# Kernel optimization log

Measured on AMD Instinct MI355X. Metric: run time of the kernel, lower is better.

Reference implementation:

```python
import jax, jax.numpy as jnp
import numpy as np
from jax import lax

EPS = 1e-6

def _class_wise_pool(x, g):
    # torch ClassWisePool: average groups of g consecutive channels
    b, c, h, w = x.shape
    return x.reshape(b, c // g, g, h, w).mean(axis=2)

def _conv1x1(wgt, bias, t):
    return jnp.einsum('oi,bihw->bohw', wgt, t) + bias[None, :, None, None]

def setup_inputs() -> dict:
    key = jax.random.key(0)
    ks = jax.random.split(key, 13)
    B, H, W = 64, 14, 14
    f = lambda k, s, sc=1.0: jax.random.normal(k, s, dtype=jnp.float32) * sc
    return {
        'r5': f(ks[0], (B, 2048, H, W)),
        'fc0_w': f(ks[1], (512, 2048, 3, 3), 0.01),
        'bn_gamma': 1.0 + 0.1 * f(ks[2], (512,)),
        'bn_beta': 0.1 * f(ks[3], (512,)),
        'bn_mean': 0.1 * f(ks[4], (512,)),
        'bn_var': 0.5 + jax.random.uniform(ks[5], (512,), dtype=jnp.float32),
        'mu0': f(ks[6], (512, 8)),
        'conv4_w': f(ks[7], (2048, 4096), 0.02),
        'conv4_b': jnp.zeros((2048,), jnp.float32),
        'down_w': f(ks[8], (32, 2048), 0.02),
        'down_b': jnp.zeros((32,), jnp.float32),
        'cls_w': f(ks[9], (8, 4096), 0.02),
        'cls_b': jnp.zeros((8,), jnp.float32),
    }

def reference(r5, fc0_w, bn_gamma, bn_beta, bn_mean, bn_var, mu0,
              conv4_w, conv4_b, down_w, down_b, cls_w, cls_b):
    B, _, H, W = r5.shape
    N = H * W
    K = 8  # emotional categories

    # fc0: Conv3x3 -> BN(eval) -> ReLU, 2048 -> 512
    y = lax.conv_general_dilated(r5, fc0_w, (1, 1), ((1, 1), (1, 1)),
                                 dimension_numbers=('NCHW', 'OIHW', 'NCHW'))
    y = (y - bn_mean[:, None, None]) * (bn_gamma / jnp.sqrt(bn_var + 1e-5))[:, None, None] + bn_beta[:, None, None]
    y = jax.nn.relu(y)

    # CAE / EM attention (EMANet-style), stage_num = 3
    x = y.reshape(B, 512, N)
    mu = mu0 / (jnp.linalg.norm(mu0, axis=0, keepdims=True) + EPS)  # [512, K]
    mu = jnp.broadcast_to(mu[None], (B, 512, K))
    z = None
    for _ in range(3):
        z = jax.nn.softmax(jnp.einsum('bcn,bck->bnk', x, mu), axis=-1)  # [B,N,K]
        zn = z / (z.sum(axis=1, keepdims=True) + EPS)
        mu = jnp.einsum('bcn,bnk->bck', x, zn)
        mu = mu / (jnp.linalg.norm(mu, axis=1, keepdims=True) + EPS)
    x_r = jnp.einsum('bck,bnk->bcn', mu, z)
    x2 = jax.nn.relu(x + x_r).reshape(B, 512, H, W)  # GCEM output
    z_t = z.transpose(0, 2, 1).reshape(B, K, H, W)   # attention map

    # class_att = z_t.view(b,8,1,h,w).mean(2) == z_t
    # per-class matmul loop + 8 cats -> single einsum, channel order i-major
    x1 = jnp.einsum('bchw,bkwv->bkchv', x2, z_t).reshape(B, K * 512, H, W)

    dic_global = _conv1x1(conv4_w, conv4_b, x1)             # [B,2048,H,W]
    xb = jnp.concatenate([r5 * dic_global, r5], axis=1)     # [B,4096,H,W]
    xb = _conv1x1(conv4_w, conv4_b, xb)                     # same conv4 reused

    xd = _conv1x1(down_w, down_b, xb)                       # downconv [B,32,H,W]
    xg = _class_wise_pool(xd.mean(axis=(2, 3), keepdims=True), 4).reshape(B, 8)  # GAP + pool
    xc = _class_wise_pool(xd, 4) * xg[:, :, None, None]     # [B,8,H,W]
    xc = _class_wise_pool(xc, 8)                            # [B,1,H,W]

    # 2047 sequential torch.cat == broadcast to 2048 channels
    xcopy = jnp.broadcast_to(xc, (B, 2048, H, W)) * r5
    xcopy = jnp.concatenate([r5, xcopy], axis=1).mean(axis=(2, 3))  # GAP -> [B,4096]
    out2 = xcopy @ cls_w.T + cls_b
    return (xg, out2)
```

## Files before the change

kernel.cpp:

```cpp
#include <hip/hip_runtime.h>
#include <hip/hip_bf16.h>

typedef unsigned short u16;
typedef unsigned int   u32;
typedef __attribute__((ext_vector_type(4))) float f32x4;
typedef __attribute__((ext_vector_type(8))) short s16x8;

__device__ __forceinline__ float b2f(u16 u){ u32 x = ((u32)u) << 16; return __builtin_bit_cast(float, x); }
__device__ __forceinline__ u16 f2b(float f){
  u32 x = __builtin_bit_cast(u32, f);
  u32 r = (x + 0x7FFFu + ((x >> 16) & 1u)) >> 16;
  return (u16)r;
}
__device__ __forceinline__ float inld(const void* p, size_t i, int isbf){
  return isbf ? b2f(((const u16*)p)[i]) : ((const float*)p)[i];
}
__device__ __forceinline__ u16 inld16(const void* p, size_t i, int isbf){
  return isbf ? ((const u16*)p)[i] : f2b(((const float*)p)[i]);
}

__global__ __launch_bounds__(256) void detect_kernel(const u32* __restrict__ r5w, int* __restrict__ flag){
  __shared__ int cnt[2];
  int t = threadIdx.x;
  if (t < 2) cnt[t] = 0;
  __syncthreads();
  int inw = 0, nz = 0;
  for (int i = t; i < 16384; i += 256){
    u32 w = r5w[i];
    if (w == 0u) continue;
    u32 e = (w >> 7) & 0xFFu;
    nz++;
    if (e >= 0x58u && e <= 0x98u) inw++;
  }
  atomicAdd(&cnt[0], inw);
  atomicAdd(&cnt[1], nz);
  __syncthreads();
  if (t == 0) flag[0] = (2 * cnt[0] >= cnt[1]) ? 1 : 0;
}

__global__ __launch_bounds__(256) void prep_kernel(
    const void* __restrict__ g, const void* __restrict__ be,
    const void* __restrict__ mn, const void* __restrict__ vr,
    const void* __restrict__ dw, const void* __restrict__ db,
    const void* __restrict__ b4, const int* __restrict__ flag,
    float* __restrict__ scale, float* __restrict__ bias,
    u16* __restrict__ dwp, float* __restrict__ dbp,
    u16* __restrict__ b4c, u16* __restrict__ zrow)
{
  const int isbf = *flag;
  int idx = blockIdx.x * 256 + threadIdx.x;
  if (idx < 512){
    float s = inld(g, idx, isbf) / sqrtf(inld(vr, idx, isbf) + 1e-5f);
    scale[idx] = s;
    bias[idx]  = inld(be, idx, isbf) - inld(mn, idx, isbf) * s;
  }
  if (idx < 128) dbp[idx] = (idx < 32) ? inld(db, idx, isbf) : 0.f;
  if (idx < 2048){
    zrow[idx] = 0;
    b4c[idx] = inld16(b4, idx, isbf);
  }
  if (idx < 128 * 2048){
    int j = idx >> 11;
    dwp[idx] = (j < 32) ? inld16(dw, idx, isbf) : (u16)0;
  }
}

__global__ __launch_bounds__(256) void wt_pack(const void* __restrict__ w, const int* __restrict__ flag,
                                               u16* __restrict__ wt){
  const int isbf = *flag;
  int idx = blockIdx.x * 256 + threadIdx.x;
  if (idx >= 512 * 18432) return;
  int o = idx / 18432;
  int r = idx - o * 18432;
  int tap = r >> 11, i = r & 2047;
  wt[idx] = inld16(w, ((size_t)(o * 2048 + i)) * 9 + tap, isbf);
}

__global__ __launch_bounds__(256) void cvt_w4(const void* __restrict__ w4, const int* __restrict__ flag,
                                              u16* __restrict__ w4c){
  const int isbf = *flag;
  int idx = blockIdx.x * 256 + threadIdx.x;
  if (idx < 2048 * 4096) w4c[idx] = inld16(w4, idx, isbf);
}

__global__ __launch_bounds__(256) void transpose_r5(const void* __restrict__ r5, size_t elem_off,
                                                    const int* __restrict__ flag, u16* __restrict__ r5nk){
  __shared__ u16 tile[64 * 197];
  const int isbf = *flag;
  int blk = blockIdx.x;
  int b = blk >> 5, c0 = (blk & 31) * 64;
  int t = threadIdx.x;
  size_t src = elem_off + ((size_t)b * 2048 + c0) * 196;
  for (int q = t; q < 64 * 196; q += 256){
    int cl = q / 196, hv = q - cl * 196;
    tile[cl * 197 + hv] = inld16(r5, src + q, isbf);
  }
  __syncthreads();
  for (int q = t; q < 64 * 196; q += 256){
    int hv = q >> 6, cl = q & 63;
    r5nk[((size_t)b * 196 + hv) * 2048 + c0 + cl] = tile[cl * 197 + hv];
  }
}

template<int MODE>
__global__ __launch_bounds__(256) void gemm_bt(
    const u16* __restrict__ Aptr, const u16* __restrict__ A2,
    const u16* __restrict__ Bw, void* __restrict__ Cout,
    const float* __restrict__ sc, const float* __restrict__ bi,
    const u16* __restrict__ bias16, const u16* __restrict__ zrow,
    int K, int ldA, int Mrows)
{
  __shared__ u16 As[128 * 32];
  __shared__ u16 Bs[128 * 32];
  const int tid = threadIdx.x;
  const int wv = tid >> 6, ln = tid & 63;
  const int m0 = blockIdx.x * 128;
  const int o0 = blockIdx.y * 128;

  const int row0 = tid >> 2;
  const int row1 = row0 + 64;
  const int kk = (tid & 3) * 8;

  int mAr[2];
  mAr[0] = m0 + row0; mAr[1] = m0 + row1;
  #pragma unroll
  for (int s = 0; s < 2; s++) if (mAr[s] >= Mrows) mAr[s] = Mrows - 1;

  int hA[2], vA[2];
  if constexpr (MODE == 0){
    #pragma unroll
    for (int s = 0; s < 2; s++){
      int hv = mAr[s] % 196;
      hA[s] = hv / 14; vA[s] = hv - hA[s] * 14;
    }
  }
  const u16* Brow0 = Bw + (size_t)(o0 + row0) * K + kk;
  const u16* Brow1 = Bw + (size_t)(o0 + row1) * K + kk;

  const int wm = (wv >> 1) * 64, wn = (wv & 1) * 64;
  const int fl = ln & 15, fq = ln >> 4;

  f32x4 acc[4][4];
  #pragma unroll
  for (int i = 0; i < 4; i++)
    #pragma unroll
    for (int j = 0; j < 4; j++) acc[i][j] = (f32x4){0.f, 0.f, 0.f, 0.f};

  for (int k0 = 0; k0 < K; k0 += 32){
    const u16 *ga0, *ga1;
    if constexpr (MODE == 0){
      int tap = k0 >> 11;
      int kin = (k0 & 2047) + kk;
      int dy = tap / 3 - 1, dx = tap - (tap / 3) * 3 - 1;
      int dlt = dy * 14 + dx;
      bool ok0 = ((unsigned)(hA[0] + dy) < 14u) && ((unsigned)(vA[0] + dx) < 14u);
      bool ok1 = ((unsigned)(hA[1] + dy) < 14u) && ((unsigned)(vA[1] + dx) < 14u);
      ga0 = ok0 ? Aptr + (size_t)(mAr[0] + dlt) * 2048 + kin : zrow + kk;
      ga1 = ok1 ? Aptr + (size_t)(mAr[1] + dlt) * 2048 + kin : zrow + kk;
    } else if constexpr (MODE == 2){
      const u16* base = (k0 < 2048) ? Aptr : A2;
      int kin = (k0 & 2047) + kk;
      ga0 = base + (size_t)mAr[0] * 2048 + kin;
      ga1 = base + (size_t)mAr[1] * 2048 + kin;
    } else {
      ga0 = Aptr + (size_t)mAr[0] * ldA + k0 + kk;
      ga1 = Aptr + (size_t)mAr[1] * ldA + k0 + kk;
    }
    uint4 a0 = *(const uint4*)ga0;
    uint4 a1 = *(const uint4*)ga1;
    uint4 b0 = *(const uint4*)(Brow0 + k0);
    uint4 b1 = *(const uint4*)(Brow1 + k0);

    __syncthreads();
    *(uint4*)&As[row0 * 32 + kk] = a0;
    *(uint4*)&As[row1 * 32 + kk] = a1;
    *(uint4*)&Bs[row0 * 32 + kk] = b0;
    *(uint4*)&Bs[row1 * 32 + kk] = b1;
    __syncthreads();

    s16x8 af[4], bfr[4];
    #pragma unroll
    for (int i = 0; i < 4; i++)
      af[i] = *(const s16x8*)&As[(wm + i * 16 + fl) * 32 + fq * 8];
    #pragma unroll
    for (int j = 0; j < 4; j++)
      bfr[j] = *(const s16x8*)&Bs[(wn + j * 16 + fl) * 32 + fq * 8];
    #pragma unroll
    for (int i = 0; i < 4; i++)
      #pragma unroll
      for (int j = 0; j < 4; j++)
        acc[i][j] = __builtin_amdgcn_mfma_f32_16x16x32_bf16(af[i], bfr[j], acc[i][j], 0, 0, 0);
  }

  #pragma unroll
  for (int i = 0; i < 4; i++){
    int mrow = m0 + wm + i * 16 + fq * 4;
    #pragma unroll
    for (int j = 0; j < 4; j++){
      int o = o0 + wn + j * 16 + fl;
      f32x4 a = acc[i][j];
      #pragma unroll
      for (int r = 0; r < 4; r++){
        int n = mrow + r;
        if (n >= Mrows) continue;
        float v = a[r];
        if constexpr (MODE == 0){
          v = fmaxf(v * sc[o] + bi[o], 0.f);
          ((u16*)Cout)[(size_t)n * 512 + o] = f2b(v);
        } else if constexpr (MODE == 1){
          v += b2f(bias16[o]);
          v *= b2f(A2[(size_t)n * 2048 + o]);
          ((u16*)Cout)[(size_t)n * 2048 + o] = f2b(v);
        } else if constexpr (MODE == 2){
          v += b2f(bias16[o]);
          ((u16*)Cout)[(size_t)n * 2048 + o] = f2b(v);
        } else {
          ((float*)Cout)[(size_t)n * 128 + o] = v + bi[o];
        }
      }
    }
  }
}

__global__ __launch_bounds__(512) void em_kernel(
    const u16* __restrict__ x, const void* __restrict__ mu0, const int* __restrict__ flag,
    u16* __restrict__ x2, float* __restrict__ zg)
{
  __shared__ float mu[512][8];
  __shared__ float zz[196][8];
  __shared__ float part[64][8];
  __shared__ float red8[8];
  const int isbf = *flag;
  const int b = blockIdx.x;
  const int t = threadIdx.x;
  const u16* xb = x + (size_t)b * 196 * 512;

  for (int q = t; q < 4096; q += 512) mu[q >> 3][q & 7] = inld(mu0, q, isbf);
  __syncthreads();
  { int k = t & 7, g = t >> 3; float s = 0;
    for (int c = g; c < 512; c += 64){ float m = mu[c][k]; s += m * m; }
    part[g][k] = s; }
  __syncthreads();
  if (t < 8){ float s = 0; for (int g = 0; g < 64; g++) s += part[g][t]; red8[t] = sqrtf(s) + 1e-6f; }
  __syncthreads();
  for (int q = t; q < 4096; q += 512) mu[q >> 3][q & 7] /= red8[q & 7];
  __syncthreads();

  for (int it = 0; it < 3; it++){
    for (int p = t; p < 1568; p += 512){
      int n = p >> 3, k = p & 7;
      const u16* xr = xb + n * 512;
      float s = 0;
      for (int c = 0; c < 512; c += 8){
        uint4 u = *(const uint4*)(xr + c);
        s += b2f((u16)(u.x & 0xffff)) * mu[c][k]     + b2f((u16)(u.x >> 16)) * mu[c + 1][k]
           + b2f((u16)(u.y & 0xffff)) * mu[c + 2][k] + b2f((u16)(u.y >> 16)) * mu[c + 3][k]
           + b2f((u16)(u.z & 0xffff)) * mu[c + 4][k] + b2f((u16)(u.z >> 16)) * mu[c + 5][k]
           + b2f((u16)(u.w & 0xffff)) * mu[c + 6][k] + b2f((u16)(u.w >> 16)) * mu[c + 7][k];
      }
      zz[n][k] = s;
    }
    __syncthreads();
    if (t < 196){
      float mx = zz[t][0];
      #pragma unroll
      for (int k = 1; k < 8; k++) mx = fmaxf(mx, zz[t][k]);
      float e[8], sm = 0;
      #pragma unroll
      for (int k = 0; k < 8; k++){ e[k] = expf(zz[t][k] - mx); sm += e[k]; }
      #pragma unroll
      for (int k = 0; k < 8; k++) zz[t][k] = e[k] / sm;
    }
    __syncthreads();
    { int k = t & 7, g = t >> 3; float s = 0;
      for (int n = g; n < 196; n += 64) s += zz[n][k];
      part[g][k] = s; }
    __syncthreads();
    if (t < 8){ float s = 0; for (int g = 0; g < 64; g++) s += part[g][t]; red8[t] = s + 1e-6f; }
    __syncthreads();
    for (int q = t; q < 4096; q += 512){
      int c = q >> 3, k = q & 7;
      float s = 0;
      for (int n = 0; n < 196; n++) s += b2f(xb[n * 512 + c]) * zz[n][k];
      mu[c][k] = s / red8[k];
    }
    __syncthreads();
    { int k = t & 7, g = t >> 3; float s = 0;
      for (int c = g; c < 512; c += 64){ float m = mu[c][k]; s += m * m; }
      part[g][k] = s; }
    __syncthreads();
    if (t < 8){ float s = 0; for (int g = 0; g < 64; g++) s += part[g][t]; red8[t] = sqrtf(s) + 1e-6f; }
    __syncthreads();
    for (int q = t; q < 4096; q += 512) mu[q >> 3][q & 7] /= red8[q & 7];
    __syncthreads();
  }

  for (int p = t; p < 1568; p += 512) zg[b * 1568 + p] = zz[p >> 3][p & 7];
  for (int q = t; q < 196 * 512; q += 512){
    int n = q >> 9, c = q & 511;
    float xr = 0;
    #pragma unroll
    for (int k = 0; k < 8; k++) xr += mu[c][k] * zz[n][k];
    float v = b2f(xb[n * 512 + c]) + xr;
    x2[(size_t)b * 196 * 512 + q] = f2b(fmaxf(v, 0.f));
  }
}

__global__ __launch_bounds__(256) void expand_kernel(
    const u16* __restrict__ x2, const float* __restrict__ zg, u16* __restrict__ x1)
{
  __shared__ u16 xs[14 * 512];
  __shared__ float zb[196 * 8];
  int bh = blockIdx.x;
  int b = bh / 14, h = bh - b * 14;
  int t = threadIdx.x;
  const u16* src = x2 + ((size_t)b * 196 + h * 14) * 512;
  for (int q = t; q < 14 * 512; q += 256) xs[q] = src[q];
  for (int q = t; q < 1568; q += 256) zb[q] = zg[b * 1568 + q];
  __syncthreads();
  size_t outbase = ((size_t)b * 196 + h * 14) * 4096;
  for (int q = t; q < 14 * 4096; q += 256){
    int v = q >> 12, kc = q & 4095;
    int k = kc >> 9, c = kc & 511;
    float s = 0;
    #pragma unroll
    for (int w = 0; w < 14; w++)
      s += b2f(xs[w * 512 + c]) * zb[(w * 14 + v) * 8 + k];
    x1[outbase + q] = f2b(s);
  }
}

__global__ __launch_bounds__(256) void pool_xg(
    const float* __restrict__ xd, const int* __restrict__ flag,
    float* __restrict__ g32, void* __restrict__ outbase, int elem_off)
{
  __shared__ float part[8][32];
  int b = blockIdx.x, t = threadIdx.x;
  int j = t & 31, g = t >> 5;
  float s = 0;
  for (int hv = g; hv < 196; hv += 8)
    s += xd[((size_t)b * 196 + hv) * 128 + j];
  part[g][j] = s;
  __syncthreads();
  if (t < 32){
    float s2 = 0;
    #pragma unroll
    for (int g2 = 0; g2 < 8; g2++) s2 += part[g2][t];
    part[0][t] = s2 * (1.f / 196.f);
  }
  __syncthreads();
  if (t < 8){
    float v = 0.25f * (part[0][4 * t] + part[0][4 * t + 1] + part[0][4 * t + 2] + part[0][4 * t + 3]);
    g32[b * 8 + t] = v;
    int o = elem_off + b * 8 + t;
    if (*flag) ((u16*)outbase)[o] = f2b(v);
    else       ((float*)outbase)[o] = v;
  }
}

__global__ __launch_bounds__(256) void final_kernel(
    const float* __restrict__ xd, const float* __restrict__ g32,
    const u16* __restrict__ r5nk, const void* __restrict__ clsw,
    const void* __restrict__ clsb, const int* __restrict__ flag,
    void* __restrict__ outbase, int elem_off)
{
  __shared__ float xc[196];
  __shared__ float red[8];
  const int isbf = *flag;
  int b = blockIdx.x, t = threadIdx.x;
  if (t < 196){
    float s = 0;
    const float* row = xd + ((size_t)b * 196 + t) * 128;
    #pragma unroll
    for (int j = 0; j < 32; j++) s += row[j] * g32[b * 8 + (j >> 2)];
    xc[t] = s * (1.f / 32.f);
  }
  if (t < 8) red[t] = 0.f;
  __syncthreads();
  float s1[8], s2[8];
  #pragma unroll
  for (int ci = 0; ci < 8; ci++){ s1[ci] = 0.f; s2[ci] = 0.f; }
  for (int hv = 0; hv < 196; hv++){
    const u16* row = r5nk + ((size_t)b * 196 + hv) * 2048;
    float xcv = xc[hv];
    #pragma unroll
    for (int ci = 0; ci < 8; ci++){
      float v = b2f(row[t + ci * 256]);
      s1[ci] += v; s2[ci] += v * xcv;
    }
  }
  float pm[8];
  #pragma unroll
  for (int m = 0; m < 8; m++) pm[m] = 0.f;
  #pragma unroll
  for (int ci = 0; ci < 8; ci++){
    int c = t + ci * 256;
    float a1 = s1[ci] * (1.f / 196.f), a2 = s2[ci] * (1.f / 196.f);
    #pragma unroll
    for (int m = 0; m < 8; m++)
      pm[m] += inld(clsw, m * 4096 + c, isbf) * a1 + inld(clsw, m * 4096 + 2048 + c, isbf) * a2;
  }
  #pragma unroll
  for (int m = 0; m < 8; m++) atomicAdd(&red[m], pm[m]);
  __syncthreads();
  if (t < 8){
    float v = red[t] + inld(clsb, t, isbf);
    int o = elem_off + b * 8 + t;
    if (isbf) ((u16*)outbase)[o] = f2b(v);
    else      ((float*)outbase)[o] = v;
  }
}

extern "C" void kernel_launch(void* const* d_in, const int* in_sizes, int n_in,
                              void* d_out, int out_size, void* d_ws, size_t ws_size,
                              hipStream_t stream)
{
  (void)in_sizes; (void)n_in; (void)out_size;
  const void* r5  = d_in[0];
  const void* fcw = d_in[1];
  const void* bng = d_in[2];
  const void* bnb = d_in[3];
  const void* bnm = d_in[4];
  const void* bnv = d_in[5];
  const void* mu0 = d_in[6];
  const void* w4  = d_in[7];
  const void* b4  = d_in[8];
  const void* dw  = d_in[9];
  const void* db  = d_in[10];
  const void* cw  = d_in[11];
  const void* cb  = d_in[12];

  auto foot = [](int nb)->size_t{
    return 42ull * 1024 * 1024 + (size_t)nb * 3670016ull;
  };
  int NB = 4;
  if (foot(64) <= ws_size) NB = 64;
  else if (foot(32) <= ws_size) NB = 32;
  else if (foot(16) <= ws_size) NB = 16;
  else if (foot(8) <= ws_size) NB = 8;
  const int rowsP = NB * 196;
  const int tiles = (rowsP + 127) / 128;
  const int passes = 64 / NB;

  char* base = (char*)d_ws;
  size_t off = 0;
  auto take = [&](size_t bytes)->char*{
    char* r = base + off;
    off = (off + bytes + 255) & ~(size_t)255;
    return r;
  };

  int*   flag = (int*)  take(256);
  float* scale= (float*)take(512 * 4);
  float* bias = (float*)take(512 * 4);
  float* dbp  = (float*)take(128 * 4);
  u16*   zrow = (u16*)  take(2048 * 2);
  u16*   b4c  = (u16*)  take(2048 * 2);
  float* g32  = (float*)take(64 * 8 * 4);
  u16*   dwp  = (u16*)  take(128 * 2048 * 2);
  float* zg   = (float*)take(64ULL * 1568 * 4);
  u16*   Wt   = (u16*)  take(512ULL * 18432 * 2);
  u16*   w4c  = (u16*)  take(2048ULL * 4096 * 2);
  u16*   r5nk = (u16*)  take((size_t)rowsP * 2048 * 2);
  u16*   regX = (u16*)  take((size_t)rowsP * 4096 * 2);
  u16*   bufC = (u16*)  take((size_t)rowsP * 2048 * 2);
  u16*   x2b  = (u16*)  take((size_t)rowsP * 512 * 2);
  float* xd   = (float*)take((size_t)rowsP * 128 * 4);

  u16* x1  = regX;
  u16* c2  = regX;
  u16* xnk = bufC;
  u16* xbA = bufC;

  detect_kernel<<<1, 256, 0, stream>>>((const u32*)r5, flag);
  prep_kernel<<<1024, 256, 0, stream>>>(bng, bnb, bnm, bnv, dw, db, b4, flag,
                                        scale, bias, dwp, dbp, b4c, zrow);
  wt_pack<<<(512 * 18432 + 255) / 256, 256, 0, stream>>>(fcw, flag, Wt);
  cvt_w4<<<(2048 * 4096) / 256, 256, 0, stream>>>(w4, flag, w4c);

  for (int p = 0; p < passes; p++){
    size_t r5off = (size_t)p * NB * 2048 * 196;
    int oxg = p * NB * 8;
    int oo2 = 512 + p * NB * 8;

    transpose_r5<<<NB * 32, 256, 0, stream>>>(r5, r5off, flag, r5nk);
    gemm_bt<0><<<dim3(tiles, 4), 256, 0, stream>>>(r5nk, nullptr, Wt, xnk, scale, bias, nullptr, zrow, 18432, 2048, rowsP);
    em_kernel<<<NB, 512, 0, stream>>>(xnk, mu0, flag, x2b, zg);
    expand_kernel<<<NB * 14, 256, 0, stream>>>(x2b, zg, x1);
    gemm_bt<1><<<dim3(tiles, 16), 256, 0, stream>>>(x1, r5nk, w4c, xbA, nullptr, nullptr, b4c, zrow, 4096, 4096, rowsP);
    gemm_bt<2><<<dim3(tiles, 16), 256, 0, stream>>>(xbA, r5nk, w4c, c2, nullptr, nullptr, b4c, zrow, 4096, 2048, rowsP);
    gemm_bt<3><<<dim3(tiles, 1), 256, 0, stream>>>(c2, nullptr, dwp, xd, nullptr, dbp, nullptr, zrow, 2048, 2048, rowsP);
    pool_xg<<<NB, 256, 0, stream>>>(xd, flag, g32, d_out, oxg);
    final_kernel<<<NB, 256, 0, stream>>>(xd, g32, r5nk, cw, cb, flag, d_out, oo2);
  }
}
```

Baseline: 1.944 ms.

## Use direct global-to-LDS loads in GEMM, swap grid order, optimize EM mu update

The GEMM tile loads now go straight from global memory into LDS through global_load_lds, instead of staging through registers, with a barrier added after the MFMA loop. For the two conv4 GEMMs the grid is transposed so that consecutive blocks walk the output-channel dimension, which changes L2 reuse of activation rows. In em_kernel each thread now accumulates all 8 clusters for one channel, so every x element is read once rather than 8 times, and the shared arrays are padded to 9 columns to avoid bank conflicts. The new LDS layout depends on global_load_lds writing lanes contiguously per wave, which has to match the row-major fragment reads; if it does not, the results are wrong.

```diff
diff --git a/kernel.cpp b/kernel.cpp
--- a/kernel.cpp
+++ b/kernel.cpp
@@ -17,6 +17,11 @@
 }
 __device__ __forceinline__ u16 inld16(const void* p, size_t i, int isbf){
   return isbf ? ((const u16*)p)[i] : f2b(((const float*)p)[i]);
+}
+
+__device__ __forceinline__ void async16(const void* g, void* l){
+  __builtin_amdgcn_global_load_lds((const __attribute__((address_space(1))) void*)g,
+                                   (__attribute__((address_space(3))) void*)l, 16, 0, 0);
 }
 
 __global__ __launch_bounds__(256) void detect_kernel(const u32* __restrict__ r5w, int* __restrict__ flag){
@@ -110,32 +115,26 @@
     const u16* __restrict__ bias16, const u16* __restrict__ zrow,
     int K, int ldA, int Mrows)
 {
+  constexpr bool SWAPG = (MODE == 1 || MODE == 2);
   __shared__ u16 As[128 * 32];
   __shared__ u16 Bs[128 * 32];
   const int tid = threadIdx.x;
   const int wv = tid >> 6, ln = tid & 63;
-  const int m0 = blockIdx.x * 128;
-  const int o0 = blockIdx.y * 128;
-
-  const int row0 = tid >> 2;
-  const int row1 = row0 + 64;
-  const int kk = (tid & 3) * 8;
-
-  int mAr[2];
-  mAr[0] = m0 + row0; mAr[1] = m0 + row1;
-  #pragma unroll
-  for (int s = 0; s < 2; s++) if (mAr[s] >= Mrows) mAr[s] = Mrows - 1;
-
-  int hA[2], vA[2];
+  const int m0 = (SWAPG ? blockIdx.y : blockIdx.x) * 128;
+  const int o0 = (SWAPG ? blockIdx.x : blockIdx.y) * 128;
+
+  const int rowA0 = wv * 32 + (ln >> 2);
+  const int kofs  = (ln & 3) * 8;
+  int mA0 = m0 + rowA0, mA1 = mA0 + 16;
+  if (mA0 >= Mrows) mA0 = Mrows - 1;
+  if (mA1 >= Mrows) mA1 = Mrows - 1;
+  const int oB0 = o0 + rowA0, oB1 = oB0 + 16;
+
+  int h0 = 0, v0 = 0, h1 = 0, v1 = 0;
   if constexpr (MODE == 0){
-    #pragma unroll
-    for (int s = 0; s < 2; s++){
-      int hv = mAr[s] % 196;
-      hA[s] = hv / 14; vA[s] = hv - hA[s] * 14;
-    }
-  }
-  const u16* Brow0 = Bw + (size_t)(o0 + row0) * K + kk;
-  const u16* Brow1 = Bw + (size_t)(o0 + row1) * K + kk;
+    int hv0 = mA0 % 196; h0 = hv0 / 14; v0 = hv0 - h0 * 14;
+    int hv1 = mA1 % 196; h1 = hv1 / 14; v1 = hv1 - h1 * 14;
+  }
 
   const int wm = (wv >> 1) * 64, wn = (wv & 1) * 64;
   const int fl = ln & 15, fq = ln >> 4;
@@ -145,37 +144,39 @@
   for (int i = 0; i < 4; i++)
     #pragma unroll
     for (int j = 0; j < 4; j++) acc[i][j] = (f32x4){0.f, 0.f, 0.f, 0.f};
+
+  u16* ldsA0 = &As[wv * 1024];
+  u16* ldsA1 = &As[wv * 1024 + 512];
+  u16* ldsB0 = &Bs[wv * 1024];
+  u16* ldsB1 = &Bs[wv * 1024 + 512];
 
   for (int k0 = 0; k0 < K; k0 += 32){
     const u16 *ga0, *ga1;
     if constexpr (MODE == 0){
       int tap = k0 >> 11;
-      int kin = (k0 & 2047) + kk;
+      int kin = (k0 & 2047) + kofs;
       int dy = tap / 3 - 1, dx = tap - (tap / 3) * 3 - 1;
       int dlt = dy * 14 + dx;
-      bool ok0 = ((unsigned)(hA[0] + dy) < 14u) && ((unsigned)(vA[0] + dx) < 14u);
-      bool ok1 = ((unsigned)(hA[1] + dy) < 14u) && ((unsigned)(vA[1] + dx) < 14u);
-      ga0 = ok0 ? Aptr + (size_t)(mAr[0] + dlt) * 2048 + kin : zrow + kk;
-      ga1 = ok1 ? Aptr + (size_t)(mAr[1] + dlt) * 2048 + kin : zrow + kk;
+      bool ok0 = ((unsigned)(h0 + dy) < 14u) && ((unsigned)(v0 + dx) < 14u);
+      bool ok1 = ((unsigned)(h1 + dy) < 14u) && ((unsigned)(v1 + dx) < 14u);
+      ga0 = ok0 ? Aptr + (size_t)(mA0 + dlt) * 2048 + kin : zrow + kofs;
+      ga1 = ok1 ? Aptr + (size_t)(mA1 + dlt) * 2048 + kin : zrow + kofs;
     } else if constexpr (MODE == 2){
       const u16* base = (k0 < 2048) ? Aptr : A2;
-      int kin = (k0 & 2047) + kk;
-      ga0 = base + (size_t)mAr[0] * 2048 + kin;
-      ga1 = base + (size_t)mAr[1] * 2048 + kin;
+      int kin = (k0 & 2047) + kofs;
+      ga0 = base + (size_t)mA0 * 2048 + kin;
+      ga1 = base + (size_t)mA1 * 2048 + kin;
     } else {
-      ga0 = Aptr + (size_t)mAr[0] * ldA + k0 + kk;
-      ga1 = Aptr + (size_t)mAr[1] * ldA + k0 + kk;
+      ga0 = Aptr + (size_t)mA0 * ldA + k0 + kofs;
+      ga1 = Aptr + (size_t)mA1 * ldA + k0 + kofs;
     }
-    uint4 a0 = *(const uint4*)ga0;
-    uint4 a1 = *(const uint4*)ga1;
-    uint4 b0 = *(const uint4*)(Brow0 + k0);
-    uint4 b1 = *(const uint4*)(Brow1 + k0);
-
-    __syncthreads();
-    *(uint4*)&As[row0 * 32 + kk] = a0;
-    *(uint4*)&As[row1 * 32 + kk] = a1;
-    *(uint4*)&Bs[row0 * 32 + kk] = b0;
-    *(uint4*)&Bs[row1 * 32 + kk] = b1;
+    const u16* gb0 = Bw + (size_t)oB0 * K + k0 + kofs;
+    const u16* gb1 = Bw + (size_t)oB1 * K + k0 + kofs;
+
+    async16(ga0, ldsA0);
+    async16(ga1, ldsA1);
+    async16(gb0, ldsB0);
+    async16(gb1, ldsB1);
     __syncthreads();
 
     s16x8 af[4], bfr[4];
@@ -190,6 +191,7 @@
       #pragma unroll
       for (int j = 0; j < 4; j++)
         acc[i][j] = __builtin_amdgcn_mfma_f32_16x16x32_bf16(af[i], bfr[j], acc[i][j], 0, 0, 0);
+    __syncthreads();
   }
 
   #pragma unroll
@@ -226,8 +228,8 @@
     const u16* __restrict__ x, const void* __restrict__ mu0, const int* __restrict__ flag,
     u16* __restrict__ x2, float* __restrict__ zg)
 {
-  __shared__ float mu[512][8];
-  __shared__ float zz[196][8];
+  __shared__ float mu[512][9];
+  __shared__ float zz[196][9];
   __shared__ float part[64][8];
   __shared__ float red8[8];
   const int isbf = *flag;
@@ -278,11 +280,19 @@
     __syncthreads();
     if (t < 8){ float s = 0; for (int g = 0; g < 64; g++) s += part[g][t]; red8[t] = s + 1e-6f; }
     __syncthreads();
-    for (int q = t; q < 4096; q += 512){
-      int c = q >> 3, k = q & 7;
-      float s = 0;
-      for (int n = 0; n < 196; n++) s += b2f(xb[n * 512 + c]) * zz[n][k];
-      mu[c][k] = s / red8[k];
+    {
+      int c = t;
+      float s[8];
+      #pragma unroll
+      for (int k = 0; k < 8; k++) s[k] = 0.f;
+      for (int n = 0; n < 196; n++){
+        float xv = b2f(xb[n * 512 + c]);
+        #pragma unroll
+        for (int k = 0; k < 8; k++) s[k] += xv * zz[n][k];
+      }
+      __syncthreads();
+      #pragma unroll
+      for (int k = 0; k < 8; k++) mu[c][k] = s[k] / red8[k];
     }
     __syncthreads();
     { int k = t & 7, g = t >> 3; float s = 0;
@@ -487,8 +497,8 @@
     gemm_bt<0><<<dim3(tiles, 4), 256, 0, stream>>>(r5nk, nullptr, Wt, xnk, scale, bias, nullptr, zrow, 18432, 2048, rowsP);
     em_kernel<<<NB, 512, 0, stream>>>(xnk, mu0, flag, x2b, zg);
     expand_kernel<<<NB * 14, 256, 0, stream>>>(x2b, zg, x1);
-    gemm_bt<1><<<dim3(tiles, 16), 256, 0, stream>>>(x1, r5nk, w4c, xbA, nullptr, nullptr, b4c, zrow, 4096, 4096, rowsP);
-    gemm_bt<2><<<dim3(tiles, 16), 256, 0, stream>>>(xbA, r5nk, w4c, c2, nullptr, nullptr, b4c, zrow, 4096, 2048, rowsP);
+    gemm_bt<1><<<dim3(16, tiles), 256, 0, stream>>>(x1, r5nk, w4c, xbA, nullptr, nullptr, b4c, zrow, 4096, 4096, rowsP);
+    gemm_bt<2><<<dim3(16, tiles), 256, 0, stream>>>(xbA, r5nk, w4c, c2, nullptr, nullptr, b4c, zrow, 4096, 2048, rowsP);
     gemm_bt<3><<<dim3(tiles, 1), 256, 0, stream>>>(c2, nullptr, dwp, xd, nullptr, dbp, nullptr, zrow, 2048, 2048, rowsP);
     pool_xg<<<NB, 256, 0, stream>>>(xd, flag, g32, d_out, oxg);
     final_kernel<<<NB, 256, 0, stream>>>(xd, g32, r5nk, cw, cb, flag, d_out, oo2);
```

Measured after the change: 1.836 ms. 5.6% less time.
